# Kernel optimization log

Hardware: AMD Instinct MI355X
Metric: run time of the kernel (lower is better)

## Reference

```python
import jax, jax.numpy as jnp
import numpy as np

MASK_THRESHOLD = 0.5
NO_OVERLAP = True


def setup_inputs() -> dict:
    key = jax.random.key(0)
    B, N, C, M = 2, 50, 80, 28
    H, W = 800, 1333
    k1, k2, k3, k4, k5, k6, k7 = jax.random.split(key, 7)
    mask_outs = jax.random.uniform(k1, (B, N, C, M, M), dtype=jnp.float32)
    # valid xyxy boxes inside the image, 20-220 px per side
    cx = jax.random.uniform(k2, (B, N), dtype=jnp.float32) * W
    cy = jax.random.uniform(k3, (B, N), dtype=jnp.float32) * H
    bw = jax.random.uniform(k4, (B, N), dtype=jnp.float32) * 200.0 + 20.0
    bh = jax.random.uniform(k5, (B, N), dtype=jnp.float32) * 200.0 + 20.0
    boxes = jnp.stack([cx - bw / 2, cy - bh / 2, cx + bw / 2, cy + bh / 2], axis=-1)
    scores = jax.random.uniform(k6, (B, N), dtype=jnp.float32)
    class_ids = jax.random.randint(k7, (B, N), 0, C).astype(jnp.int64)
    return {"mask_outs": mask_outs, "boxes": boxes, "scores": scores,
            "class_ids": class_ids, "orig_h": H, "orig_w": W}


def _gather_rows(m, idx, size):
    # m: [Mh, Mw], idx: [L] int32 -> [L, Mw], zero outside [0, size)
    valid = (idx >= 0) & (idx < size)
    v = m[jnp.clip(idx, 0, size - 1)]
    return v * valid[:, None].astype(m.dtype)


def _gather_cols(m, idx, size):
    # m: [H, Mw], idx: [L] int32 -> [H, L], zero outside [0, size)
    valid = (idx >= 0) & (idx < size)
    v = m[:, jnp.clip(idx, 0, size - 1)]
    return v * valid[None, :].astype(m.dtype)


def _paste_soft(masks, boxes, H, W):
    # Equivalent to torch grid_sample(align_corners=False, zeros padding) on the
    # affine grid built from boxes (detectron2 _do_paste_mask), exploiting the
    # separable (outer-product) structure of the grid.
    # masks: [N, Mh, Mw], boxes: [N, 4] -> [N, H, W] float
    N, Mh, Mw = masks.shape
    x0, y0, x1, y1 = (boxes[:, 0:1], boxes[:, 1:2], boxes[:, 2:3], boxes[:, 3:4])
    img_y = jnp.arange(H, dtype=masks.dtype) + 0.5  # [H]
    img_x = jnp.arange(W, dtype=masks.dtype) + 0.5  # [W]
    gy = (img_y[None, :] - y0) / (y1 - y0) * 2.0 - 1.0  # [N, H] normalized
    gx = (img_x[None, :] - x0) / (x1 - x0) * 2.0 - 1.0  # [N, W]
    iy = ((gy + 1.0) * Mh - 1.0) / 2.0  # unnormalize, align_corners=False
    ix = ((gx + 1.0) * Mw - 1.0) / 2.0
    # --- bilinear along y: [N, Mh, Mw] -> [N, H, Mw]
    iy0 = jnp.floor(iy)
    wy = (iy - iy0)[..., None]
    iy0i = iy0.astype(jnp.int32)
    ry0 = jax.vmap(_gather_rows, in_axes=(0, 0, None))(masks, iy0i, Mh)
    ry1 = jax.vmap(_gather_rows, in_axes=(0, 0, None))(masks, iy0i + 1, Mh)
    rows = ry0 * (1.0 - wy) + ry1 * wy  # [N, H, Mw]
    # --- bilinear along x: [N, H, Mw] -> [N, H, W]
    ix0 = jnp.floor(ix)
    wx = (ix - ix0)[:, None, :]
    ix0i = ix0.astype(jnp.int32)
    cx0 = jax.vmap(_gather_cols, in_axes=(0, 0, None))(rows, ix0i, Mw)
    cx1 = jax.vmap(_gather_cols, in_axes=(0, 0, None))(rows, ix0i + 1, Mw)
    return cx0 * (1.0 - wx) + cx1 * wx  # [N, H, W]


def _remove_overlap(masks, scores):
    # Highest-scoring mask claims each pixel (matches sequential fg-suppression).
    order = jnp.argsort(-scores)
    sm = masks[order].astype(jnp.int32)  # [N, H, W]
    prev_cover = jnp.cumsum(sm, axis=0) - sm  # masks covering pixel before i
    keep = (sm > 0) & (prev_cover == 0)
    inv = jnp.argsort(order)
    return keep[inv]


def reference(mask_outs, boxes, scores, class_ids, orig_h, orig_w):
    # select class-specific mask: [B, N, C, M, M] -> [B, N, M, M]
    idx = class_ids.astype(jnp.int32)[:, :, None, None, None]
    sel = jnp.take_along_axis(mask_outs, idx, axis=2)[:, :, 0]
    soft = jax.vmap(lambda m, b: _paste_soft(m, b, orig_h, orig_w))(sel, boxes)
    masks = soft >= MASK_THRESHOLD  # [B, N, H, W] bool
    if NO_OVERLAP:
        masks = jax.vmap(_remove_overlap)(masks, scores)
    return masks, scores, class_ids
```

## Files before the change

kernel.cpp:

```cpp
#include <hip/hip_runtime.h>

#define NDET 50
#define BN   100
#define NC   80
#define MM   28
#define IMH  800
#define IMW  1333
#define HW   (IMH * IMW)

struct Params {
    float ylo, yhi, xlo, xhi;
    float y0, x0, dh, dw;
    float score;
    int   base;
};

__global__ void det2mask_setup(const float* __restrict__ boxes,
                               const float* __restrict__ scores,
                               const int*   __restrict__ class_ids,
                               Params* __restrict__ ps,
                               float* __restrict__ out_tail) {
#pragma clang fp contract(off)
    int i = threadIdx.x;
    if (i < BN) {
        float x0 = boxes[i * 4 + 0];
        float y0 = boxes[i * 4 + 1];
        float x1 = boxes[i * 4 + 2];
        float y1 = boxes[i * 4 + 3];
        float dw = x1 - x0;
        float dh = y1 - y0;
        Params p;
        p.y0 = y0; p.x0 = x0; p.dh = dh; p.dw = dw;
        p.ylo = y0 - dh * (0.5f / 28.0f) - 1.0f;
        p.yhi = y1 + dh * (0.5f / 28.0f) + 1.0f;
        p.xlo = x0 - dw * (0.5f / 28.0f) - 1.0f;
        p.xhi = x1 + dw * (0.5f / 28.0f) + 1.0f;
        p.score = scores[i];
        int cls = class_ids[i];
        p.base = (i * NC + cls) * (MM * MM);
        ps[i] = p;
        out_tail[i]      = scores[i];
        out_tail[BN + i] = (float)cls;
    }
}

__global__ __launch_bounds__(128) void det2mask_main(
        const float* __restrict__ mask_outs,
        const Params* __restrict__ ps,
        float* __restrict__ out) {
#pragma clang fp contract(off)
    __shared__ float s_xlo[NDET], s_xhi[NDET], s_x0[NDET], s_dw[NDET];
    __shared__ float s_sc[NDET], s_wy[NDET];
    __shared__ int   s_rb0[NDET], s_rb1[NDET], s_n[NDET];
    __shared__ int   s_ns;

    const int b = blockIdx.z;
    const int y = blockIdx.y;
    const float py = (float)y + 0.5f;
    const int tid = threadIdx.x;

    if (tid < 64) {
        bool cov = false;
        Params p;
        if (tid < NDET) {
            p = ps[b * NDET + tid];
            cov = (py > p.ylo) && (py < p.yhi);
        }
        unsigned long long m = __ballot(cov);
        if (cov) {
            int pos = __popcll(m & ((1ull << tid) - 1ull));
            float gy = (py - p.y0) / p.dh * 2.0f - 1.0f;
            float iy = ((gy + 1.0f) * 28.0f - 1.0f) / 2.0f;
            float fy = floorf(iy);
            float wy = iy - fy;
            int iy0 = (int)fy;
            bool r0 = (iy0 >= 0) && (iy0 <= MM - 1);
            bool r1 = (iy0 >= -1) && (iy0 <= MM - 2);
            int yc0 = min(max(iy0, 0), MM - 1);
            int yc1 = min(max(iy0 + 1, 0), MM - 1);
            s_xlo[pos] = p.xlo; s_xhi[pos] = p.xhi;
            s_x0[pos] = p.x0;   s_dw[pos] = p.dw;
            s_sc[pos] = p.score; s_wy[pos] = wy;
            s_rb0[pos] = r0 ? (p.base + yc0 * MM) : -1;
            s_rb1[pos] = r1 ? (p.base + yc1 * MM) : -1;
            s_n[pos] = tid;
        }
        if (tid == 0) s_ns = __popcll(m);
    }
    __syncthreads();

    const int ns = s_ns;
    const int sOff = (4 - (y & 3)) & 3;
    const int nq = (IMW - sOff) >> 2;
    const int t = blockIdx.x * 128 + tid;

    int xs, cnt;
    bool vec = false;
    if (t < nq)            { xs = sOff + 4 * t;  cnt = 4;         vec = true; }
    else if (t == nq)      { xs = sOff + 4 * nq; cnt = IMW - xs;  }
    else if (t == nq + 1)  { xs = 0;             cnt = sOff;      }
    else                   { xs = 0;             cnt = 0;         }

    int best[4] = {-1, -1, -1, -1};
    if (cnt > 0) {
        float bs[4] = {-1.0f, -1.0f, -1.0f, -1.0f};
        const float qlo = (float)xs + 0.5f;
        const float qhi = (float)(xs + cnt - 1) + 0.5f;
        for (int s2 = 0; s2 < ns; ++s2) {
            float xlo = s_xlo[s2], xhi = s_xhi[s2];
            if (qhi <= xlo || qlo >= xhi) continue;
            float x0 = s_x0[s2], dw = s_dw[s2];
            float wy = s_wy[s2], sc = s_sc[s2];
            int rb0 = s_rb0[s2], rb1 = s_rb1[s2];
            int n = s_n[s2];
#pragma unroll
            for (int k = 0; k < 4; ++k) {
                if (k >= cnt) break;
                float px = (float)(xs + k) + 0.5f;
                if (px <= xlo || px >= xhi) continue;
                float gx = (px - x0) / dw * 2.0f - 1.0f;
                float ix = ((gx + 1.0f) * 28.0f - 1.0f) / 2.0f;
                float fx = floorf(ix);
                float wx = ix - fx;
                int ix0 = (int)fx;
                bool c0 = (ix0 >= 0) && (ix0 <= MM - 1);
                bool c1 = (ix0 >= -1) && (ix0 <= MM - 2);
                int xc0 = min(max(ix0, 0), MM - 1);
                int xc1 = min(max(ix0 + 1, 0), MM - 1);
                float v00 = (rb0 >= 0 && c0) ? mask_outs[rb0 + xc0] : 0.0f;
                float v10 = (rb1 >= 0 && c0) ? mask_outs[rb1 + xc0] : 0.0f;
                float v01 = (rb0 >= 0 && c1) ? mask_outs[rb0 + xc1] : 0.0f;
                float v11 = (rb1 >= 0 && c1) ? mask_outs[rb1 + xc1] : 0.0f;
                float rr0 = v00 * (1.0f - wy) + v10 * wy;
                float rr1 = v01 * (1.0f - wy) + v11 * wy;
                float val = rr0 * (1.0f - wx) + rr1 * wx;
                if (val >= 0.5f && sc > bs[k]) { bs[k] = sc; best[k] = n; }
            }
        }
    }

    if (cnt > 0) {
        float* op = out + (size_t)b * NDET * HW + (size_t)y * IMW + xs;
        if (vec) {
            for (int n = 0; n < NDET; ++n) {
                float4 v;
                v.x = (best[0] == n) ? 1.0f : 0.0f;
                v.y = (best[1] == n) ? 1.0f : 0.0f;
                v.z = (best[2] == n) ? 1.0f : 0.0f;
                v.w = (best[3] == n) ? 1.0f : 0.0f;
                *reinterpret_cast<float4*>(op) = v;
                op += HW;
            }
        } else {
            for (int n = 0; n < NDET; ++n) {
#pragma unroll
                for (int k = 0; k < 3; ++k) {
                    if (k < cnt) op[k] = (best[k] == n) ? 1.0f : 0.0f;
                }
                op += HW;
            }
        }
    }
}

extern "C" void kernel_launch(void* const* d_in, const int* in_sizes, int n_in,
                              void* d_out, int out_size, void* d_ws, size_t ws_size,
                              hipStream_t stream) {
    const float* mask_outs = (const float*)d_in[0];
    const float* boxes     = (const float*)d_in[1];
    const float* scores    = (const float*)d_in[2];
    const int*   class_ids = (const int*)d_in[3];
    float* out = (float*)d_out;
    Params* ps = (Params*)d_ws;

    hipLaunchKernelGGL(det2mask_setup, dim3(1), dim3(128), 0, stream,
                       boxes, scores, class_ids, ps, out + (size_t)BN * HW);

    dim3 grid(3, IMH, 2);
    hipLaunchKernelGGL(det2mask_main, grid, dim3(128), 0, stream,
                       mask_outs, ps, out);
}
```

Baseline: 513.5 us.

## Split mask paste into byte-index winner pass and plane-wise float expansion

The main kernel now computes only the winning detection index per pixel and stores it as one byte in workspace, using one 384-thread block per row instead of three 128-thread blocks. A second kernel expands that byte map into the 100 float output planes, writing each plane contiguously with float4 stores. The aim is to replace the strided 50-plane write loop in each thread with streaming, plane-contiguous writes. The cost is an extra launch plus a byte-map write and reread.

```diff
diff --git a/kernel.cpp b/kernel.cpp
--- a/kernel.cpp
+++ b/kernel.cpp
@@ -7,6 +7,7 @@
 #define IMH  800
 #define IMW  1333
 #define HW   (IMH * IMW)
+#define NQ_PLANE (HW / 4)
 
 struct Params {
     float ylo, yhi, xlo, xhi;
@@ -44,10 +45,10 @@
     }
 }
 
-__global__ __launch_bounds__(128) void det2mask_main(
+__global__ __launch_bounds__(384) void det2mask_best(
         const float* __restrict__ mask_outs,
         const Params* __restrict__ ps,
-        float* __restrict__ out) {
+        unsigned char* __restrict__ best8) {
 #pragma clang fp contract(off)
     __shared__ float s_xlo[NDET], s_xhi[NDET], s_x0[NDET], s_dw[NDET];
     __shared__ float s_sc[NDET], s_wy[NDET];
@@ -92,14 +93,13 @@
     const int ns = s_ns;
     const int sOff = (4 - (y & 3)) & 3;
     const int nq = (IMW - sOff) >> 2;
-    const int t = blockIdx.x * 128 + tid;
 
     int xs, cnt;
     bool vec = false;
-    if (t < nq)            { xs = sOff + 4 * t;  cnt = 4;         vec = true; }
-    else if (t == nq)      { xs = sOff + 4 * nq; cnt = IMW - xs;  }
-    else if (t == nq + 1)  { xs = 0;             cnt = sOff;      }
-    else                   { xs = 0;             cnt = 0;         }
+    if (tid < nq)            { xs = sOff + 4 * tid; cnt = 4;        vec = true; }
+    else if (tid == nq)      { xs = sOff + 4 * nq;  cnt = IMW - xs; }
+    else if (tid == nq + 1)  { xs = 0;              cnt = sOff;     }
+    else                     { xs = 0;              cnt = 0;        }
 
     int best[4] = {-1, -1, -1, -1};
     if (cnt > 0) {
@@ -140,25 +140,42 @@
     }
 
     if (cnt > 0) {
-        float* op = out + (size_t)b * NDET * HW + (size_t)y * IMW + xs;
+        unsigned char* bp = best8 + (size_t)b * HW + (size_t)y * IMW + xs;
         if (vec) {
-            for (int n = 0; n < NDET; ++n) {
-                float4 v;
-                v.x = (best[0] == n) ? 1.0f : 0.0f;
-                v.y = (best[1] == n) ? 1.0f : 0.0f;
-                v.z = (best[2] == n) ? 1.0f : 0.0f;
-                v.w = (best[3] == n) ? 1.0f : 0.0f;
-                *reinterpret_cast<float4*>(op) = v;
-                op += HW;
+            unsigned int v = (unsigned int)(best[0] & 0xFF)
+                           | ((unsigned int)(best[1] & 0xFF) << 8)
+                           | ((unsigned int)(best[2] & 0xFF) << 16)
+                           | ((unsigned int)(best[3] & 0xFF) << 24);
+            *reinterpret_cast<unsigned int*>(bp) = v;
+        } else {
+#pragma unroll
+            for (int k = 0; k < 3; ++k) {
+                if (k < cnt) bp[k] = (unsigned char)(best[k] & 0xFF);
             }
-        } else {
-            for (int n = 0; n < NDET; ++n) {
+        }
+    }
+}
+
+__global__ __launch_bounds__(256) void det2mask_write(
+        const unsigned char* __restrict__ best8,
+        float* __restrict__ out) {
+    const int pid = blockIdx.y;
+    const int b = (pid >= NDET) ? 1 : 0;
+    const int n = pid - b * NDET;
+    const unsigned int* bp = reinterpret_cast<const unsigned int*>(best8 + (size_t)b * HW);
+    float4* op = reinterpret_cast<float4*>(out + (size_t)pid * HW);
+    const int q0 = blockIdx.x * 1024 + threadIdx.x;
 #pragma unroll
-                for (int k = 0; k < 3; ++k) {
-                    if (k < cnt) op[k] = (best[k] == n) ? 1.0f : 0.0f;
-                }
-                op += HW;
-            }
+    for (int i = 0; i < 4; ++i) {
+        int q = q0 + i * 256;
+        if (q < NQ_PLANE) {
+            unsigned int v = bp[q];
+            float4 f;
+            f.x = (((v      ) & 0xFFu) == (unsigned)n) ? 1.0f : 0.0f;
+            f.y = (((v >>  8) & 0xFFu) == (unsigned)n) ? 1.0f : 0.0f;
+            f.z = (((v >> 16) & 0xFFu) == (unsigned)n) ? 1.0f : 0.0f;
+            f.w = (((v >> 24) & 0xFFu) == (unsigned)n) ? 1.0f : 0.0f;
+            op[q] = f;
         }
     }
 }
@@ -172,11 +189,15 @@
     const int*   class_ids = (const int*)d_in[3];
     float* out = (float*)d_out;
     Params* ps = (Params*)d_ws;
+    unsigned char* best8 = (unsigned char*)d_ws + 4096;
 
     hipLaunchKernelGGL(det2mask_setup, dim3(1), dim3(128), 0, stream,
                        boxes, scores, class_ids, ps, out + (size_t)BN * HW);
 
-    dim3 grid(3, IMH, 2);
-    hipLaunchKernelGGL(det2mask_main, grid, dim3(128), 0, stream,
-                       mask_outs, ps, out);
-}
+    hipLaunchKernelGGL(det2mask_best, dim3(1, IMH, 2), dim3(384), 0, stream,
+                       mask_outs, ps, best8);
+
+    dim3 gw((NQ_PLANE + 1023) / 1024, BN);
+    hipLaunchKernelGGL(det2mask_write, gw, dim3(256), 0, stream,
+                       best8, out);
+}
```

After: 451.0 us. 1.14x faster.
